# Kernel tuning notes

Measured on AMD Instinct MI355X. Metric: run time of the kernel, lower is better.

Reference implementation:

```python
import jax, jax.numpy as jnp
import numpy as np

NUM_HEADS = 8
AREA = 4
EPS = 1e-5  # torch BatchNorm2d default


def _conv1x1(x, w):
    # x: [B,C,H,W], w: [O,C] -> [B,O,H,W]
    return jnp.einsum('bchw,oc->bohw', x, w)


def _bn(y, g, b, m, v):
    # inference-mode BatchNorm2d, per-channel affine
    s = g / jnp.sqrt(v + EPS)
    return y * s[None, :, None, None] + (b - m * s)[None, :, None, None]


def setup_inputs() -> dict:
    key = jax.random.key(0)
    ks = jax.random.split(key, 16)
    B, C, H, W = 2, 256, 64, 64
    d = {}
    d['x'] = jax.random.normal(ks[0], (B, C, H, W), jnp.float32)
    # qk conv (dim -> 2*dim) + BN
    d['w_qk'] = jax.random.normal(ks[1], (2 * C, C), jnp.float32) * 0.06
    d['g_qk'] = jax.random.uniform(ks[2], (2 * C,), jnp.float32, 0.5, 1.5)
    d['b_qk'] = jax.random.normal(ks[3], (2 * C,), jnp.float32) * 0.1
    d['m_qk'] = jax.random.normal(ks[4], (2 * C,), jnp.float32) * 0.1
    d['v_qk'] = jax.random.uniform(ks[5], (2 * C,), jnp.float32, 0.5, 1.5)
    # v conv (dim -> dim) + BN
    d['w_v'] = jax.random.normal(ks[6], (C, C), jnp.float32) * 0.06
    d['g_v'] = jax.random.uniform(ks[7], (C,), jnp.float32, 0.5, 1.5)
    d['b_v'] = jax.random.normal(ks[8], (C,), jnp.float32) * 0.1
    d['m_v'] = jax.random.normal(ks[9], (C,), jnp.float32) * 0.1
    d['v_v'] = jax.random.uniform(ks[10], (C,), jnp.float32, 0.5, 1.5)
    # proj conv (dim -> dim) + BN
    d['w_p'] = jax.random.normal(ks[11], (C, C), jnp.float32) * 0.06
    d['g_p'] = jax.random.uniform(ks[12], (C,), jnp.float32, 0.5, 1.5)
    d['b_p'] = jax.random.normal(ks[13], (C,), jnp.float32) * 0.1
    d['m_p'] = jax.random.normal(ks[14], (C,), jnp.float32) * 0.1
    d['v_p'] = jax.random.uniform(ks[15], (C,), jnp.float32, 0.5, 1.5)
    return d


def reference(x, w_qk, g_qk, b_qk, m_qk, v_qk,
              w_v, g_v, b_v, m_v, v_v,
              w_p, g_p, b_p, m_p, v_p):
    B, C, H, W = x.shape
    N = H * W
    hd = C // NUM_HEADS

    qk = _bn(_conv1x1(x, w_qk), g_qk, b_qk, m_qk, v_qk)          # [B,2C,H,W]
    qk = qk.reshape(B, 2 * C, N).transpose(0, 2, 1)               # [B,N,2C]
    vv = _bn(_conv1x1(x, w_v), g_v, b_v, m_v, v_v)                # [B,C,H,W]
    vv = vv.reshape(B, C, N).transpose(0, 2, 1)                   # [B,N,C]

    Ba, Na = B * AREA, N // AREA
    qk = qk.reshape(Ba, Na, 2 * C)
    vv = vv.reshape(Ba, Na, C)
    q, k = qk[..., :C], qk[..., C:]

    # [Ba,Na,C] -> [Ba,heads,hd,Na] (matches torch transpose(1,2).view)
    q = q.reshape(Ba, Na, NUM_HEADS, hd).transpose(0, 2, 3, 1)
    k = k.reshape(Ba, Na, NUM_HEADS, hd).transpose(0, 2, 3, 1)
    v = vv.reshape(Ba, Na, NUM_HEADS, hd).transpose(0, 2, 3, 1)

    scale = hd ** -0.5
    attn = jnp.einsum('bhdi,bhdj->bhij', q, k) * scale            # [Ba,h,Na,Na]
    attn = jax.nn.softmax(attn, axis=-1)                          # max-sub exp/sum
    out = jnp.einsum('bhdj,bhij->bihd', v, attn)                  # [Ba,Na,h,hd]

    out = out.reshape(B, N, C).reshape(B, H, W, C).transpose(0, 3, 1, 2)
    return _bn(_conv1x1(out, w_p), g_p, b_p, m_p, v_p)            # [B,C,H,W]
```

## Files before the change

kernel.cpp:

```cpp
#include <hip/hip_runtime.h>
#include <hip/hip_bf16.h>
#include <math.h>

#define CCH   256
#define NPIX  4096
#define NHD   8
#define HD    32
#define NA    1024
#define BN_EPS 1e-5f
#define ATT_SCALE (0.17677669529663687f * 1.4426950408889634f)

typedef __attribute__((ext_vector_type(8))) short bf16x8;
typedef __attribute__((ext_vector_type(4))) short bf16x4;
typedef __attribute__((ext_vector_type(4))) float f32x4;

static __device__ inline short f2bf(float f) {
    union { float f; unsigned u; } v; v.f = f;
    unsigned r = (v.u + 0x7fff + ((v.u >> 16) & 1)) >> 16;
    return (short)r;
}

static __device__ inline unsigned int pk2bf(float a, float b) {
    __hip_bfloat162 h2 = __float22bfloat162_rn(make_float2(a, b));
    union { __hip_bfloat162 h; unsigned int u; } v; v.h = h2;
    return v.u;
}

__global__ __launch_bounds__(256)
void prep_kernel(const float* __restrict__ x, short* __restrict__ Xt,
                 const float* __restrict__ wqk, const float* __restrict__ wv,
                 const float* __restrict__ wp, short* __restrict__ Wb) {
    __shared__ short tile[64][66];
    const int t = threadIdx.x;
    const int z = blockIdx.z;
    if (z == 2) {
        const int id  = blockIdx.y * 64 + blockIdx.x;
        const int idx = (id * 256 + t) * 4;
        const float* src; int off;
        if (idx < 131072)      { src = wqk; off = idx; }
        else if (idx < 196608) { src = wv;  off = idx - 131072; }
        else                   { src = wp;  off = idx - 196608; }
        const float4 v = *(const float4*)(src + off);
        short4 o;
        o.x = f2bf(v.x); o.y = f2bf(v.y); o.z = f2bf(v.z); o.w = f2bf(v.w);
        *(short4*)(Wb + idx) = o;
        return;
    }
    const int n0 = blockIdx.x << 6;
    const int c0 = blockIdx.y << 6;
    const int b  = z;
    const float* xp = x + (((size_t)(b * CCH + c0)) << 12) + n0;
    #pragma unroll
    for (int j = 0; j < 16; ++j) {
        const int lin = (j << 8) + t;
        const int cl = lin >> 6, nl = lin & 63;
        tile[cl][nl] = f2bf(xp[((size_t)cl << 12) + nl]);
    }
    __syncthreads();
    short* xtp = Xt + ((((size_t)b << 12) + n0) << 8) + c0;
    #pragma unroll
    for (int j = 0; j < 16; ++j) {
        const int lin = (j << 8) + t;
        const int nl = lin >> 6, cl = lin & 63;
        xtp[((size_t)nl << 8) + cl] = tile[cl][nl];
    }
}

__global__ __launch_bounds__(256)
void qkv_gemm(const short* __restrict__ Xt, const short* __restrict__ Wb,
              const float* __restrict__ g_qk, const float* __restrict__ b_qk,
              const float* __restrict__ m_qk, const float* __restrict__ v_qk,
              const float* __restrict__ g_v, const float* __restrict__ b_v,
              const float* __restrict__ m_v, const float* __restrict__ v_v,
              short* __restrict__ Qb, short* __restrict__ Kb,
              short* __restrict__ Vb) {
    __shared__ short A_lds[128][72];
    __shared__ short B_lds[64][72];
    const int t    = threadIdx.x;
    const int lane = t & 63;
    const int w    = t >> 6;
    const int c    = lane & 15;
    const int quad = lane >> 4;
    const int wm   = w >> 1;
    const int wn   = w & 1;
    const int m0 = blockIdx.x * 128;
    const int n0 = blockIdx.y * 64 + wn * 32;

    const int rowS = t >> 3;
    const int kc   = t & 7;
    const short* gA0 = Xt + (size_t)(m0 + rowS) * 256 + kc * 8;
    const short* gA1 = gA0 + 32 * 256;
    const short* gA2 = gA0 + 64 * 256;
    const short* gA3 = gA0 + 96 * 256;
    const short* gB0 = Wb + (size_t)(blockIdx.y * 64 + rowS) * 256 + kc * 8;
    const short* gB1 = gB0 + 32 * 256;
    short* lA0 = &A_lds[rowS][kc * 8];
    short* lA1 = &A_lds[rowS + 32][kc * 8];
    short* lA2 = &A_lds[rowS + 64][kc * 8];
    short* lA3 = &A_lds[rowS + 96][kc * 8];
    short* lB0 = &B_lds[rowS][kc * 8];
    short* lB1 = &B_lds[rowS + 32][kc * 8];

    f32x4 acc[4][2];
    #pragma unroll
    for (int f = 0; f < 4; ++f)
        #pragma unroll
        for (int g = 0; g < 2; ++g) acc[f][g] = (f32x4){0.f, 0.f, 0.f, 0.f};

    #pragma unroll
    for (int kt = 0; kt < 4; ++kt) {
        const int k0 = kt * 64;
        bf16x8 a0 = *(const bf16x8*)(gA0 + k0);
        bf16x8 a1 = *(const bf16x8*)(gA1 + k0);
        bf16x8 a2 = *(const bf16x8*)(gA2 + k0);
        bf16x8 a3 = *(const bf16x8*)(gA3 + k0);
        bf16x8 b0 = *(const bf16x8*)(gB0 + k0);
        bf16x8 b1 = *(const bf16x8*)(gB1 + k0);
        if (kt) __syncthreads();
        *(bf16x8*)lA0 = a0;
        *(bf16x8*)lA1 = a1;
        *(bf16x8*)lA2 = a2;
        *(bf16x8*)lA3 = a3;
        *(bf16x8*)lB0 = b0;
        *(bf16x8*)lB1 = b1;
        __syncthreads();
        #pragma unroll
        for (int s = 0; s < 2; ++s) {
            const int ko = s * 32 + quad * 8;
            bf16x8 af[4], bg[2];
            #pragma unroll
            for (int f = 0; f < 4; ++f)
                af[f] = *(const bf16x8*)&A_lds[wm * 64 + f * 16 + c][ko];
            #pragma unroll
            for (int g = 0; g < 2; ++g)
                bg[g] = *(const bf16x8*)&B_lds[wn * 32 + g * 16 + c][ko];
            #pragma unroll
            for (int f = 0; f < 4; ++f)
                #pragma unroll
                for (int g = 0; g < 2; ++g)
                    acc[f][g] = __builtin_amdgcn_mfma_f32_16x16x32_bf16(af[f], bg[g], acc[f][g], 0, 0, 0);
        }
    }

    const int mw = m0 + wm * 64;
    if (n0 < 512) {
        const bool isQ = (n0 < 256);
        short* dst = isQ ? Qb : Kb;
        const float fold = isQ ? ATT_SCALE : 1.0f;
        #pragma unroll
        for (int g = 0; g < 2; ++g) {
            const int o  = n0 + g * 16 + c;
            const int cd = o & 255;
            const int h  = cd >> 5;
            const int d  = cd & 31;
            float s    = g_qk[o] * rsqrtf(v_qk[o] + BN_EPS);
            float beta = (b_qk[o] - m_qk[o] * s) * fold;
            s *= fold;
            #pragma unroll
            for (int f = 0; f < 4; ++f) {
                #pragma unroll
                for (int r = 0; r < 4; ++r) {
                    const int row  = mw + f * 16 + (quad << 2) + r;
                    const int pair = (row >> 10) * NHD + h;
                    const int i    = row & 1023;
                    dst[(((size_t)pair << 10) + i) * HD + d] = f2bf(acc[f][g][r] * s + beta);
                }
            }
        }
    } else {
        #pragma unroll
        for (int g = 0; g < 2; ++g) {
            const int c2 = n0 + g * 16 + c - 512;
            const int d  = c2 & 31;
            const int hp = c2 >> 5;
            const float s    = g_v[c2] * rsqrtf(v_v[c2] + BN_EPS);
            const float beta = b_v[c2] - m_v[c2] * s;
            #pragma unroll
            for (int f = 0; f < 4; ++f) {
                #pragma unroll
                for (int r = 0; r < 4; ++r) {
                    const int row  = mw + f * 16 + (quad << 2) + r;
                    const int pair = (row >> 10) * NHD + hp;
                    const int j    = row & 1023;
                    Vb[((size_t)pair << 15) + (d << 10) + j] = f2bf(acc[f][g][r] * s + beta);
                }
            }
        }
    }
}

__global__ __launch_bounds__(256, 4)
void attn_kernel(const short* __restrict__ Qb,
                 const short* __restrict__ Kb,
                 const short* __restrict__ Vb,
                 short* __restrict__ AOt) {
    const int tid  = threadIdx.x;
    const int wave = tid >> 6;
    const int lane = tid & 63;
    const int c    = lane & 15;
    const int quad = lane >> 4;
    const int pidx  = wave >> 1;
    const int jhalf = wave & 1;

    const int bx  = blockIdx.x;
    const int hi  = bx >> 3;
    const int p   = (bx & 7) + ((hi >> 4) << 3);
    const int blk = hi & 15;
    const int i0a = (blk << 6) + (pidx << 5);
    const int i0b = i0a + 16;
    const int ba  = p >> 3;
    const int h   = p & 7;

    __shared__ __align__(16) short Klds[2][64][40];
    __shared__ __align__(16) short Vlds[2][32][72];
    __shared__ f32x4 mrgA[2][4][64];
    __shared__ float mrgL[2][2][64];

    const short* qbase = Qb + ((size_t)p << 15);
    const short* kbase = Kb + ((size_t)p << 15);
    const short* vbase = Vb + ((size_t)p << 15);

    bf16x8 qfa = *(const bf16x8*)(qbase + ((i0a + c) << 5) + (quad << 3));
    bf16x8 qfb = *(const bf16x8*)(qbase + ((i0b + c) << 5) + (quad << 3));

    const int krow = tid >> 2;
    const int kkc  = tid & 3;
    const int jj_  = krow >> 5;
    const int r32  = krow & 31;
    const int r16  = r32 & 15;
    const int srcr = ((r16 >> 2) << 3) + (r16 & 3) + ((r32 >> 4) << 2) + (jj_ << 5);
    const short* kS = kbase + (srcr << 5) + kkc * 8;
    short* kD0 = &Klds[0][krow][kkc * 8];
    short* kD1 = &Klds[1][krow][kkc * 8];
    const int vrow = tid >> 3;
    const int vkc  = tid & 7;
    const short* vS = vbase + (vrow << 10) + vkc * 8;
    short* vD0 = &Vlds[0][vrow][vkc * 8];
    short* vD1 = &Vlds[1][vrow][vkc * 8];

    f32x4 acc0a = {0.f,0.f,0.f,0.f}, acc1a = {0.f,0.f,0.f,0.f};
    f32x4 acc0b = {0.f,0.f,0.f,0.f}, acc1b = {0.f,0.f,0.f,0.f};
    float la = 0.f, lb = 0.f;
    const f32x4 zero = {0.f,0.f,0.f,0.f};

    for (int it = 0; it < 8; ++it) {
        const int joff = it << 6;
        bf16x8 k0 = *(const bf16x8*)(kS + (joff << 5));
        bf16x8 k1 = *(const bf16x8*)(kS + ((joff + 512) << 5));
        bf16x8 v0 = *(const bf16x8*)(vS + joff);
        bf16x8 v1 = *(const bf16x8*)(vS + joff + 512);
        if (it) __syncthreads();
        *(bf16x8*)kD0 = k0;
        *(bf16x8*)kD1 = k1;
        *(bf16x8*)vD0 = v0;
        *(bf16x8*)vD1 = v1;
        __syncthreads();

        #pragma unroll
        for (int jj = 0; jj < 2; ++jj) {
            bf16x8 kf0 = *(const bf16x8*)&Klds[jhalf][(jj << 5) + c][quad << 3];
            bf16x8 kf1 = *(const bf16x8*)&Klds[jhalf][(jj << 5) + 16 + c][quad << 3];
            bf16x8 vf0 = *(const bf16x8*)&Vlds[jhalf][c][(jj << 5) + (quad << 3)];
            bf16x8 vf1 = *(const bf16x8*)&Vlds[jhalf][c + 16][(jj << 5) + (quad << 3)];

            f32x4 s0a = __builtin_amdgcn_mfma_f32_16x16x32_bf16(kf0, qfa, zero, 0, 0, 0);
            f32x4 s1a = __builtin_amdgcn_mfma_f32_16x16x32_bf16(kf1, qfa, zero, 0, 0, 0);
            f32x4 s0b = __builtin_amdgcn_mfma_f32_16x16x32_bf16(kf0, qfb, zero, 0, 0, 0);
            f32x4 s1b = __builtin_amdgcn_mfma_f32_16x16x32_bf16(kf1, qfb, zero, 0, 0, 0);

            float p0a[4], p1a[4], p0b[4], p1b[4];
            #pragma unroll
            for (int r = 0; r < 4; ++r) {
                p0a[r] = __builtin_amdgcn_exp2f(s0a[r]);
                p1a[r] = __builtin_amdgcn_exp2f(s1a[r]);
                p0b[r] = __builtin_amdgcn_exp2f(s0b[r]);
                p1b[r] = __builtin_amdgcn_exp2f(s1b[r]);
            }
            la += (p0a[0]+p0a[1]) + (p0a[2]+p0a[3]) + (p1a[0]+p1a[1]) + (p1a[2]+p1a[3]);
            lb += (p0b[0]+p0b[1]) + (p0b[2]+p0b[3]) + (p1b[0]+p1b[1]) + (p1b[2]+p1b[3]);

            union { unsigned int u[4]; bf16x8 v; } pfa, pfb;
            pfa.u[0] = pk2bf(p0a[0], p0a[1]);
            pfa.u[1] = pk2bf(p0a[2], p0a[3]);
            pfa.u[2] = pk2bf(p1a[0], p1a[1]);
            pfa.u[3] = pk2bf(p1a[2], p1a[3]);
            pfb.u[0] = pk2bf(p0b[0], p0b[1]);
            pfb.u[1] = pk2bf(p0b[2], p0b[3]);
            pfb.u[2] = pk2bf(p1b[0], p1b[1]);
            pfb.u[3] = pk2bf(p1b[2], p1b[3]);

            acc0a = __builtin_amdgcn_mfma_f32_16x16x32_bf16(pfa.v, vf0, acc0a, 0, 0, 0);
            acc1a = __builtin_amdgcn_mfma_f32_16x16x32_bf16(pfa.v, vf1, acc1a, 0, 0, 0);
            acc0b = __builtin_amdgcn_mfma_f32_16x16x32_bf16(pfb.v, vf0, acc0b, 0, 0, 0);
            acc1b = __builtin_amdgcn_mfma_f32_16x16x32_bf16(pfb.v, vf1, acc1b, 0, 0, 0);
        }
    }

    __syncthreads();
    if (jhalf == 1) {
        mrgA[pidx][0][lane] = acc0a;
        mrgA[pidx][1][lane] = acc1a;
        mrgA[pidx][2][lane] = acc0b;
        mrgA[pidx][3][lane] = acc1b;
        mrgL[pidx][0][lane] = la;
        mrgL[pidx][1][lane] = lb;
    }
    __syncthreads();
    if (jhalf == 1) return;

    acc0a += mrgA[pidx][0][lane];
    acc1a += mrgA[pidx][1][lane];
    acc0b += mrgA[pidx][2][lane];
    acc1b += mrgA[pidx][3][lane];
    la += mrgL[pidx][0][lane];
    lb += mrgL[pidx][1][lane];

    la += __shfl_xor(la, 16); la += __shfl_xor(la, 32);
    lb += __shfl_xor(lb, 16); lb += __shfl_xor(lb, 32);

    #pragma unroll
    for (int r = 0; r < 4; ++r) {
        const int rr = (quad << 2) + r;
        const float rla = 1.f / __shfl(la, rr, 16);
        const float rlb = 1.f / __shfl(lb, rr, 16);
        const size_t basea = ((((size_t)ba << 10) + i0a + rr) << 8) + (h << 5);
        const size_t baseb = ((((size_t)ba << 10) + i0b + rr) << 8) + (h << 5);
        AOt[basea + c]      = f2bf(acc0a[r] * rla);
        AOt[basea + c + 16] = f2bf(acc1a[r] * rla);
        AOt[baseb + c]      = f2bf(acc0b[r] * rlb);
        AOt[baseb + c + 16] = f2bf(acc1b[r] * rlb);
    }
}

__global__ __launch_bounds__(256)
void pconv_gemm(const short* __restrict__ Wp, const short* __restrict__ AOt,
                const float* __restrict__ g_p, const float* __restrict__ b_p,
                const float* __restrict__ m_p, const float* __restrict__ v_p,
                float* __restrict__ out) {
    __shared__ short A_lds[64][72];
    __shared__ short B_lds[64][72];
    const int t    = threadIdx.x;
    const int lane = t & 63;
    const int w    = t >> 6;
    const int c    = lane & 15;
    const int quad = lane >> 4;
    const int wm   = w >> 1;
    const int wn   = w & 1;
    const int m0 = blockIdx.x * 64;
    const int n0 = blockIdx.y * 64;

    const int rowS = t >> 3;
    const int kc   = t & 7;
    const short* gA0 = Wp + (size_t)(m0 + rowS) * 256 + kc * 8;
    const short* gA1 = gA0 + 32 * 256;
    const short* gB0 = AOt + (size_t)(n0 + rowS) * 256 + kc * 8;
    const short* gB1 = gB0 + 32 * 256;
    short* lA0 = &A_lds[rowS][kc * 8];
    short* lA1 = &A_lds[rowS + 32][kc * 8];
    short* lB0 = &B_lds[rowS][kc * 8];
    short* lB1 = &B_lds[rowS + 32][kc * 8];

    f32x4 acc[2][2];
    #pragma unroll
    for (int f = 0; f < 2; ++f)
        #pragma unroll
        for (int g = 0; g < 2; ++g) acc[f][g] = (f32x4){0.f, 0.f, 0.f, 0.f};

    #pragma unroll
    for (int kt = 0; kt < 4; ++kt) {
        const int k0 = kt * 64;
        bf16x8 a0 = *(const bf16x8*)(gA0 + k0);
        bf16x8 a1 = *(const bf16x8*)(gA1 + k0);
        bf16x8 b0 = *(const bf16x8*)(gB0 + k0);
        bf16x8 b1 = *(const bf16x8*)(gB1 + k0);
        if (kt) __syncthreads();
        *(bf16x8*)lA0 = a0;
        *(bf16x8*)lA1 = a1;
        *(bf16x8*)lB0 = b0;
        *(bf16x8*)lB1 = b1;
        __syncthreads();
        #pragma unroll
        for (int s = 0; s < 2; ++s) {
            const int ko = s * 32 + quad * 8;
            bf16x8 af0 = *(const bf16x8*)&A_lds[wm * 32 + c][ko];
            bf16x8 af1 = *(const bf16x8*)&A_lds[wm * 32 + 16 + c][ko];
            bf16x8 bg0 = *(const bf16x8*)&B_lds[wn * 32 + c][ko];
            bf16x8 bg1 = *(const bf16x8*)&B_lds[wn * 32 + 16 + c][ko];
            acc[0][0] = __builtin_amdgcn_mfma_f32_16x16x32_bf16(af0, bg0, acc[0][0], 0, 0, 0);
            acc[0][1] = __builtin_amdgcn_mfma_f32_16x16x32_bf16(af0, bg1, acc[0][1], 0, 0, 0);
            acc[1][0] = __builtin_amdgcn_mfma_f32_16x16x32_bf16(af1, bg0, acc[1][0], 0, 0, 0);
            acc[1][1] = __builtin_amdgcn_mfma_f32_16x16x32_bf16(af1, bg1, acc[1][1], 0, 0, 0);
        }
    }

    const int mw = m0 + wm * 32;
    const int nw = n0 + wn * 32;
    #pragma unroll
    for (int f = 0; f < 2; ++f) {
        #pragma unroll
        for (int r = 0; r < 4; ++r) {
            const int o = mw + f * 16 + (quad << 2) + r;
            const float s    = g_p[o] * rsqrtf(v_p[o] + BN_EPS);
            const float beta = b_p[o] - m_p[o] * s;
            #pragma unroll
            for (int g = 0; g < 2; ++g) {
                const int col = nw + g * 16 + c;
                const int b = col >> 12, n = col & 4095;
                out[((size_t)(b * CCH + o) << 12) + n] = acc[f][g][r] * s + beta;
            }
        }
    }
}

extern "C" void kernel_launch(void* const* d_in, const int* in_sizes, int n_in,
                              void* d_out, int out_size, void* d_ws, size_t ws_size,
                              hipStream_t stream) {
    const float* x    = (const float*)d_in[0];
    const float* w_qk = (const float*)d_in[1];
    const float* g_qk = (const float*)d_in[2];
    const float* b_qk = (const float*)d_in[3];
    const float* m_qk = (const float*)d_in[4];
    const float* v_qk = (const float*)d_in[5];
    const float* w_v  = (const float*)d_in[6];
    const float* g_v  = (const float*)d_in[7];
    const float* b_v  = (const float*)d_in[8];
    const float* m_v  = (const float*)d_in[9];
    const float* v_v  = (const float*)d_in[10];
    const float* w_p  = (const float*)d_in[11];
    const float* g_p  = (const float*)d_in[12];
    const float* b_p  = (const float*)d_in[13];
    const float* m_p  = (const float*)d_in[14];
    const float* v_p  = (const float*)d_in[15];

    short* Qb  = (short*)d_ws;
    short* Kb  = Qb + 2097152;
    short* Vb  = Kb + 2097152;
    short* Xt  = Vb + 2097152;
    short* Wb  = Xt + 2097152;
    short* AOt = Xt;

    dim3 gprep(64, 4, 3);
    prep_kernel<<<gprep, 256, 0, stream>>>(x, Xt, w_qk, w_v, w_p, Wb);

    dim3 gqkv(64, 12);
    qkv_gemm<<<gqkv, 256, 0, stream>>>(Xt, Wb, g_qk, b_qk, m_qk, v_qk,
                                       g_v, b_v, m_v, v_v, Qb, Kb, Vb);

    attn_kernel<<<1024, 256, 0, stream>>>(Qb, Kb, Vb, AOt);

    dim3 gp(4, 128);
    pconv_gemm<<<gp, 256, 0, stream>>>(Wb + 768 * 256, AOt, g_p, b_p, m_p, v_p, (float*)d_out);
}
```

Baseline: 123.6 us.

## Double attention block size to share K/V LDS tiles across more query rows

The attention kernel moves from 256-thread blocks covering 64 query rows to 512-thread blocks covering 128 rows, launched as 512 blocks instead of 1024. Each K/V tile staged in LDS now feeds twice as many query rows, cutting global K/V loads per query roughly in half. Each thread loads one K and one V vector per iteration instead of two, and the merge scratch arrays grow to fit four wave pairs. The trade-off is fewer blocks to spread across the GPU, more waves waiting at each barrier, and tighter register pressure from the larger launch bound.

```diff
diff --git a/kernel.cpp b/kernel.cpp
--- a/kernel.cpp
+++ b/kernel.cpp
@@ -189,7 +189,7 @@
     }
 }
 
-__global__ __launch_bounds__(256, 4)
+__global__ __launch_bounds__(512, 4)
 void attn_kernel(const short* __restrict__ Qb,
                  const short* __restrict__ Kb,
                  const short* __restrict__ Vb,
@@ -203,18 +203,17 @@
     const int jhalf = wave & 1;
 
     const int bx  = blockIdx.x;
-    const int hi  = bx >> 3;
-    const int p   = (bx & 7) + ((hi >> 4) << 3);
-    const int blk = hi & 15;
-    const int i0a = (blk << 6) + (pidx << 5);
+    const int h   = bx & 7;
+    const int ba  = (bx >> 3) & 7;
+    const int blk = bx >> 6;
+    const int p   = ba * NHD + h;
+    const int i0a = (blk << 7) + (pidx << 5);
     const int i0b = i0a + 16;
-    const int ba  = p >> 3;
-    const int h   = p & 7;
 
     __shared__ __align__(16) short Klds[2][64][40];
     __shared__ __align__(16) short Vlds[2][32][72];
-    __shared__ f32x4 mrgA[2][4][64];
-    __shared__ float mrgL[2][2][64];
+    __shared__ f32x4 mrgA[4][4][64];
+    __shared__ float mrgL[4][2][64];
 
     const short* qbase = Qb + ((size_t)p << 15);
     const short* kbase = Kb + ((size_t)p << 15);
@@ -223,20 +222,20 @@
     bf16x8 qfa = *(const bf16x8*)(qbase + ((i0a + c) << 5) + (quad << 3));
     bf16x8 qfb = *(const bf16x8*)(qbase + ((i0b + c) << 5) + (quad << 3));
 
-    const int krow = tid >> 2;
-    const int kkc  = tid & 3;
+    const int sjh  = tid >> 8;
+    const int srem = tid & 255;
+    const int krow = srem >> 2;
+    const int kkc  = srem & 3;
     const int jj_  = krow >> 5;
     const int r32  = krow & 31;
     const int r16  = r32 & 15;
     const int srcr = ((r16 >> 2) << 3) + (r16 & 3) + ((r32 >> 4) << 2) + (jj_ << 5);
-    const short* kS = kbase + (srcr << 5) + kkc * 8;
-    short* kD0 = &Klds[0][krow][kkc * 8];
-    short* kD1 = &Klds[1][krow][kkc * 8];
-    const int vrow = tid >> 3;
-    const int vkc  = tid & 7;
-    const short* vS = vbase + (vrow << 10) + vkc * 8;
-    short* vD0 = &Vlds[0][vrow][vkc * 8];
-    short* vD1 = &Vlds[1][vrow][vkc * 8];
+    const short* kS = kbase + (((sjh << 9) + srcr) << 5) + kkc * 8;
+    short* kD = &Klds[sjh][krow][kkc * 8];
+    const int vrow = srem >> 3;
+    const int vkc  = srem & 7;
+    const short* vS = vbase + (vrow << 10) + (sjh << 9) + vkc * 8;
+    short* vD = &Vlds[sjh][vrow][vkc * 8];
 
     f32x4 acc0a = {0.f,0.f,0.f,0.f}, acc1a = {0.f,0.f,0.f,0.f};
     f32x4 acc0b = {0.f,0.f,0.f,0.f}, acc1b = {0.f,0.f,0.f,0.f};
@@ -246,14 +245,10 @@
     for (int it = 0; it < 8; ++it) {
         const int joff = it << 6;
         bf16x8 k0 = *(const bf16x8*)(kS + (joff << 5));
-        bf16x8 k1 = *(const bf16x8*)(kS + ((joff + 512) << 5));
         bf16x8 v0 = *(const bf16x8*)(vS + joff);
-        bf16x8 v1 = *(const bf16x8*)(vS + joff + 512);
         if (it) __syncthreads();
-        *(bf16x8*)kD0 = k0;
-        *(bf16x8*)kD1 = k1;
-        *(bf16x8*)vD0 = v0;
-        *(bf16x8*)vD1 = v1;
+        *(bf16x8*)kD = k0;
+        *(bf16x8*)vD = v0;
         __syncthreads();
 
         #pragma unroll
@@ -446,7 +441,7 @@
     qkv_gemm<<<gqkv, 256, 0, stream>>>(Xt, Wb, g_qk, b_qk, m_qk, v_qk,
                                        g_v, b_v, m_v, v_v, Qb, Kb, Vb);
 
-    attn_kernel<<<1024, 256, 0, stream>>>(Qb, Kb, Vb, AOt);
+    attn_kernel<<<512, 512, 0, stream>>>(Qb, Kb, Vb, AOt);
 
     dim3 gp(4, 128);
     pconv_gemm<<<gp, 256, 0, stream>>>(Wb + 768 * 256, AOt, g_p, b_p, m_p, v_p, (float*)d_out);
```

Result: no change. 125.4 us (+1.4%).
